# Kernel optimization log

Measured on AMD Instinct MI355X. Metric: run time of the kernel, lower is better.

Reference implementation:

```python
import jax, jax.numpy as jnp
import numpy as np

N_NODES = 50000
N_EDGES = 1600000
IN_DIM, HID_DIM, OUT_DIM, HEADS = 128, 128, 64, 8
NEG_SLOPE = 0.2
BN_EPS = 1e-5


def setup_inputs() -> dict:
    key = jax.random.key(0)
    ks = jax.random.split(key, 12)
    hpc = HID_DIM // HEADS  # per-head channels of layer 1
    return {
        "x": jax.random.normal(ks[0], (N_NODES, IN_DIM), jnp.float32),
        "edge_index": jax.random.randint(ks[1], (2, N_EDGES), 0, N_NODES, jnp.int64),
        "W1": jax.random.normal(ks[2], (IN_DIM, HEADS * hpc), jnp.float32) * 0.05,
        "a1_src": jax.random.normal(ks[3], (HEADS, hpc), jnp.float32) * 0.1,
        "a1_dst": jax.random.normal(ks[4], (HEADS, hpc), jnp.float32) * 0.1,
        "b1": jnp.zeros((HEADS * hpc,), jnp.float32),
        "bn_gamma": jnp.ones((HID_DIM,), jnp.float32),
        "bn_beta": jnp.zeros((HID_DIM,), jnp.float32),
        "W2": jax.random.normal(ks[5], (HID_DIM, OUT_DIM), jnp.float32) * 0.05,
        "a2_src": jax.random.normal(ks[6], (1, OUT_DIM), jnp.float32) * 0.1,
        "a2_dst": jax.random.normal(ks[7], (1, OUT_DIM), jnp.float32) * 0.1,
        "b2": jnp.zeros((OUT_DIM,), jnp.float32),
    }


def _gat_conv(x, src, dst, W, a_src, a_dst, bias, heads, n_nodes):
    # x: [N, Fin]; src/dst: [E'] (self-loops already appended)
    hpc = W.shape[1] // heads
    h = (x @ W).reshape(n_nodes, heads, hpc)                 # [N,H,C]
    alpha_s = jnp.einsum("nhc,hc->nh", h, a_src)             # [N,H]
    alpha_d = jnp.einsum("nhc,hc->nh", h, a_dst)
    e = alpha_s[src] + alpha_d[dst]                          # [E',H]
    e = jax.nn.leaky_relu(e, NEG_SLOPE)
    # segment softmax over destination neighborhoods
    m = jax.ops.segment_max(e, dst, num_segments=n_nodes)    # [N,H]
    m = jnp.where(jnp.isfinite(m), m, 0.0)
    ee = jnp.exp(e - m[dst])
    denom = jax.ops.segment_sum(ee, dst, num_segments=n_nodes)
    alpha = ee / (denom[dst] + 1e-16)                        # [E',H]
    msg = h[src] * alpha[:, :, None]                         # [E',H,C]
    out = jax.ops.segment_sum(msg, dst, num_segments=n_nodes)  # [N,H,C]
    return out.reshape(n_nodes, heads * hpc) + bias


def _batch_norm(x, gamma, beta):
    mu = jnp.mean(x, axis=0)
    var = jnp.var(x, axis=0)
    return gamma * (x - mu) * jax.lax.rsqrt(var + BN_EPS) + beta


def reference(x, edge_index, W1, a1_src, a1_dst, b1, bn_gamma, bn_beta, W2, a2_src, a2_dst, b2):
    n = x.shape[0]
    loops = jnp.arange(n, dtype=edge_index.dtype)
    src = jnp.concatenate([edge_index[0], loops])            # PyG add_self_loops
    dst = jnp.concatenate([edge_index[1], loops])
    h = _gat_conv(x, src, dst, W1, a1_src, a1_dst, b1, HEADS, n)
    h = _batch_norm(h, bn_gamma, bn_beta)
    h = jax.nn.elu(h)
    # dropout: identity at inference
    out = _gat_conv(h, src, dst, W2, a2_src, a2_dst, b2, 1, n)
    return out
```

## Files before the change

### kernel.cpp

```cpp
#include <hip/hip_runtime.h>
#include <hip/hip_bf16.h>

#define N_NODES 50000
#define N_EDGES 1600000
#define HEADS 8
#define NBK 196
#define NBLK 196

typedef unsigned short u16;
typedef unsigned int u32;
typedef __attribute__((ext_vector_type(8))) short bf16x8;
typedef __attribute__((ext_vector_type(4))) float f32x4;

__device__ __forceinline__ float bf2f(u16 u) {
  union { u32 i; float f; } v; v.i = ((u32)u) << 16; return v.f;
}
__device__ __forceinline__ float bflo(u32 p) {
  union { u32 i; float f; } v; v.i = p << 16; return v.f;
}
__device__ __forceinline__ float bfhi(u32 p) {
  union { u32 i; float f; } v; v.i = p & 0xffff0000u; return v.f;
}
__device__ __forceinline__ u16 f2bf(float f) {
  union { float f; u32 i; } v; v.f = f;
  u32 r = v.i + 0x7fff + ((v.i >> 16) & 1);
  return (u16)(r >> 16);
}
__device__ __forceinline__ u32 pack2(float a, float b) {
  return (u32)f2bf(a) | ((u32)f2bf(b) << 16);
}

__global__ void k_detect(const u16* __restrict__ x, const u32* __restrict__ ei,
                         int* __restrict__ flags) {
  __shared__ int cbig, cnz;
  if (threadIdx.x == 0) { cbig = 0; cnz = 0; }
  __syncthreads();
  int lb = 0, ln = 0;
  for (int i = threadIdx.x; i < 4096; i += 256) {
    int ex = (x[i] >> 7) & 0xff;
    lb += (ex >= 140);
    if (i < 2048) ln += (ei[2 * i + 1] != 0);
  }
  atomicAdd(&cbig, lb); atomicAdd(&cnz, ln);
  __syncthreads();
  if (threadIdx.x == 0) {
    flags[0] = (cbig > 16) ? 1 : 0;
    flags[1] = (cnz == 0) ? 1 : 0;
  }
}

__global__ void k_convsmall(const void* a1s, const void* a1d, const void* b1,
                            const void* gam, const void* bet, const void* a2s,
                            const void* a2d, const void* b2, const void* W1,
                            const void* W2, float* __restrict__ smallf,
                            u16* __restrict__ w1t, u16* __restrict__ w2t,
                            const int* __restrict__ flags) {
  int i = blockIdx.x * 256 + threadIdx.x;
  if (i >= 25408) return;
  bool f32 = flags[0] != 0;
  auto ld = [&](const void* p, int off) -> float {
    return f32 ? ((const float*)p)[off] : bf2f(((const u16*)p)[off]);
  };
  if (i >= 17216) {
    int j = i - 17216, n = j >> 7, k = j & 127;
    w2t[j] = f2bf(ld(W2, k * 64 + n));
  } else if (i >= 832) {
    int j = i - 832, n = j >> 7, k = j & 127;
    w1t[j] = f2bf(ld(W1, k * 128 + n));
  } else {
    const void* src; int off;
    if (i >= 768)      { src = b2;  off = i - 768; }
    else if (i >= 704) { src = a2d; off = i - 704; }
    else if (i >= 640) { src = a2s; off = i - 640; }
    else if (i >= 512) { src = bet; off = i - 512; }
    else if (i >= 384) { src = gam; off = i - 384; }
    else if (i >= 256) { src = b1;  off = i - 256; }
    else if (i >= 128) { src = a1d; off = i - 128; }
    else               { src = a1s; off = i; }
    smallf[i] = ld(src, off);
  }
}

__global__ __launch_bounds__(256) void k_hist(const int* __restrict__ ei,
                                              int* __restrict__ H,
                                              int* __restrict__ totals,
                                              const int* __restrict__ flags) {
  __shared__ int hist[NBK];
  int t = threadIdx.x, blk = blockIdx.x;
  for (int i = t; i < NBK; i += 256) hist[i] = 0;
  __syncthreads();
  bool i64 = flags[1] != 0;
  int base = blk * 8192;
  for (int k = 0; k < 32; k++) {
    int e = base + k * 256 + t;
    if (e < N_EDGES) {
      int d = i64 ? ei[2 * (N_EDGES + e)] : ei[N_EDGES + e];
      atomicAdd(&hist[d >> 8], 1);
    }
  }
  __syncthreads();
  for (int i = t; i < NBK; i += 256) {
    H[i * NBLK + blk] = hist[i];
    atomicAdd(&totals[i], hist[i]);
  }
}

__global__ void k_scan_tot(const int* __restrict__ totals, int* __restrict__ bucketBase) {
  __shared__ int tmp[256];
  int t = threadIdx.x;
  int v = (t < NBK) ? totals[t] : 0;
  tmp[t] = v; __syncthreads();
  for (int o = 1; o < 256; o <<= 1) {
    int x = (t >= o) ? tmp[t - o] : 0; __syncthreads();
    tmp[t] += x; __syncthreads();
  }
  if (t < NBK) bucketBase[t] = tmp[t] - v;
  if (t == NBK - 1) bucketBase[NBK] = tmp[t];
}

__global__ void k_scan_blk(const int* __restrict__ H, const int* __restrict__ bucketBase,
                           int* __restrict__ P) {
  __shared__ int tmp[256];
  int t = threadIdx.x, b = blockIdx.x;
  int v = (t < NBLK) ? H[b * NBLK + t] : 0;
  tmp[t] = v; __syncthreads();
  for (int o = 1; o < 256; o <<= 1) {
    int x = (t >= o) ? tmp[t - o] : 0; __syncthreads();
    tmp[t] += x; __syncthreads();
  }
  if (t < NBLK) P[b * NBLK + t] = bucketBase[b] + tmp[t] - v;
}

__global__ __launch_bounds__(256) void k_bucket(const int* __restrict__ ei,
                                                const int* __restrict__ P,
                                                u32* __restrict__ buf,
                                                const int* __restrict__ flags) {
  __shared__ int cur[NBK];
  int t = threadIdx.x, blk = blockIdx.x;
  for (int i = t; i < NBK; i += 256) cur[i] = P[i * NBLK + blk];
  __syncthreads();
  bool i64 = flags[1] != 0;
  int base = blk * 8192;
  for (int k = 0; k < 32; k++) {
    int e = base + k * 256 + t;
    if (e < N_EDGES) {
      int s = i64 ? ei[2 * e] : ei[e];
      int d = i64 ? ei[2 * (N_EDGES + e)] : ei[N_EDGES + e];
      int pos = atomicAdd(&cur[d >> 8], 1);
      buf[pos] = ((u32)(d & 255) << 16) | (u32)s;
    }
  }
}

__global__ __launch_bounds__(256) void k_csr(const u32* __restrict__ buf,
                                             const int* __restrict__ bucketBase,
                                             int* __restrict__ row_start,
                                             int* __restrict__ deg,
                                             int* __restrict__ csr, int N) {
  __shared__ int cnt[256], scn[256], cur[256];
  int b = blockIdx.x, t = threadIdx.x;
  int lo = bucketBase[b], hi = bucketBase[b + 1];
  cnt[t] = 0; __syncthreads();
  for (int e = lo + t; e < hi; e += 256) atomicAdd(&cnt[(buf[e] >> 16) & 255], 1);
  __syncthreads();
  int v = cnt[t];
  scn[t] = v; __syncthreads();
  for (int o = 1; o < 256; o <<= 1) {
    int x = (t >= o) ? scn[t - o] : 0; __syncthreads();
    scn[t] += x; __syncthreads();
  }
  int excl = scn[t] - v;
  int node = b * 256 + t;
  if (node < N) { row_start[node] = lo + excl; deg[node] = v; }
  cur[t] = lo + excl;
  __syncthreads();
  for (int e = lo + t; e < hi; e += 256) {
    u32 p = buf[e];
    int pos = atomicAdd(&cur[(p >> 16) & 255], 1);
    csr[pos] = p & 0xffff;
  }
}

template <int NCOLS, bool EPI, bool AFLAG>
__global__ __launch_bounds__(256) void k_gemm_mfma(const void* __restrict__ A,
                                                   const u16* __restrict__ BT,
                                                   const float* __restrict__ scale,
                                                   const float* __restrict__ shift,
                                                   u16* __restrict__ C, int M,
                                                   const int* __restrict__ flags) {
  constexpr int KP = 136;
  constexpr int NT = NCOLS / 16;
  __shared__ u16 As[64 * KP];
  __shared__ u16 Bs[NCOLS * KP];
  int t = threadIdx.x;
  int row0 = blockIdx.x * 64;
  bool af32 = AFLAG ? (flags[0] != 0) : false;

  for (int i = t; i < NCOLS * 16; i += 256) {
    int n = i >> 4, q = i & 15;
    *(uint4*)&Bs[n * KP + q * 8] = ((const uint4*)BT)[n * 16 + q];
  }
  for (int i = t; i < 64 * 32; i += 256) {
    int r = i >> 5, c4 = i & 31;
    int row = row0 + r;
    uint2 pk = make_uint2(0u, 0u);
    if (row < M) {
      if (EPI) {
        uint2 p = ((const uint2*)A)[(size_t)row * 32 + c4];
        int c = c4 * 4;
        float v0 = bflo(p.x), v1 = bfhi(p.x), v2 = bflo(p.y), v3 = bfhi(p.y);
        v0 = fmaf(v0, scale[c],     shift[c]);     v0 = v0 > 0.f ? v0 : __expf(v0) - 1.f;
        v1 = fmaf(v1, scale[c + 1], shift[c + 1]); v1 = v1 > 0.f ? v1 : __expf(v1) - 1.f;
        v2 = fmaf(v2, scale[c + 2], shift[c + 2]); v2 = v2 > 0.f ? v2 : __expf(v2) - 1.f;
        v3 = fmaf(v3, scale[c + 3], shift[c + 3]); v3 = v3 > 0.f ? v3 : __expf(v3) - 1.f;
        pk.x = pack2(v0, v1); pk.y = pack2(v2, v3);
      } else if (af32) {
        float4 v = ((const float4*)A)[(size_t)row * 32 + c4];
        pk.x = pack2(v.x, v.y); pk.y = pack2(v.z, v.w);
      } else {
        pk = ((const uint2*)A)[(size_t)row * 32 + c4];
      }
    }
    *(uint2*)&As[r * KP + c4 * 4] = pk;
  }
  __syncthreads();

  int lane = t & 63, w = t >> 6;
  int m = lane & 15, quad = lane >> 4;
  f32x4 acc[NT];
#pragma unroll
  for (int nt = 0; nt < NT; nt++) acc[nt] = (f32x4)(0.f);
  const u16* aBase = &As[(w * 16 + m) * KP + quad * 8];
  const u16* bBase = &Bs[m * KP + quad * 8];
#pragma unroll
  for (int ks = 0; ks < 4; ks++) {
    bf16x8 af = *(const bf16x8*)(aBase + ks * 32);
#pragma unroll
    for (int nt = 0; nt < NT; nt++) {
      bf16x8 bf = *(const bf16x8*)(bBase + nt * 16 * KP + ks * 32);
      acc[nt] = __builtin_amdgcn_mfma_f32_16x16x32_bf16(af, bf, acc[nt], 0, 0, 0);
    }
  }
  int orow0 = row0 + w * 16 + quad * 4;
#pragma unroll
  for (int nt = 0; nt < NT; nt++) {
#pragma unroll
    for (int r = 0; r < 4; r++) {
      int row = orow0 + r;
      if (row < M) C[(size_t)row * NCOLS + nt * 16 + m] = f2bf(acc[nt][r]);
    }
  }
}

__global__ void k_alpha1(const u16* __restrict__ h1b, const float* __restrict__ a1s,
                         const float* __restrict__ a1d, float* __restrict__ as_out,
                         float* __restrict__ ad_out, int N) {
  int idx = blockIdx.x * 256 + threadIdx.x;
  if (idx >= N * HEADS) return;
  int n = idx >> 3, h = idx & 7;
  const u32* hp = (const u32*)&h1b[((size_t)n << 7) + (h << 4)];
  float s = 0.f, d = 0.f;
#pragma unroll
  for (int q = 0; q < 8; q++) {
    u32 p = hp[q];
    float v0 = bflo(p), v1 = bfhi(p);
    int b = (h << 4) + q * 2;
    s = fmaf(v0, a1s[b], s); s = fmaf(v1, a1s[b + 1], s);
    d = fmaf(v0, a1d[b], d); d = fmaf(v1, a1d[b + 1], d);
  }
  as_out[idx] = s; ad_out[idx] = d;
}

__global__ __launch_bounds__(256) void k_agg1(const u16* __restrict__ h1b,
                                              const float* __restrict__ as_,
                                              const float* __restrict__ ad_,
                                              const int* __restrict__ csr,
                                              const int* __restrict__ row_start,
                                              const int* __restrict__ deg,
                                              const float* __restrict__ b1,
                                              u16* __restrict__ out, int N) {
  int node = blockIdx.x * 4 + (threadIdx.x >> 6);
  if (node >= N) return;
  int l = threadIdx.x & 63;
  int head = l >> 3;
  int node_u = __builtin_amdgcn_readfirstlane(node);
  int st = __builtin_amdgcn_readfirstlane(row_start[node_u]);
  int cnt = __builtin_amdgcn_readfirstlane(deg[node_u]);
  const int* cp = csr + st;
  const u32* h32 = (const u32*)h1b;
  float ad = ad_[(node_u << 3) | head];
  float s = 0.f, a0 = 0.f, a1 = 0.f;
  int j = 0;
  for (; j + 4 <= cnt; j += 4) {
    int s0 = cp[j], s1 = cp[j + 1], s2 = cp[j + 2], s3 = cp[j + 3];
    float e0 = (as_ + (s0 << 3))[head], e1 = (as_ + (s1 << 3))[head];
    float e2 = (as_ + (s2 << 3))[head], e3 = (as_ + (s3 << 3))[head];
    u32 h0 = (h32 + (s0 << 6))[l], h1v = (h32 + (s1 << 6))[l];
    u32 h2v = (h32 + (s2 << 6))[l], h3 = (h32 + (s3 << 6))[l];
    e0 += ad; e0 = fmaxf(e0, 0.2f * e0); float p0 = __expf(e0);
    e1 += ad; e1 = fmaxf(e1, 0.2f * e1); float p1 = __expf(e1);
    e2 += ad; e2 = fmaxf(e2, 0.2f * e2); float p2 = __expf(e2);
    e3 += ad; e3 = fmaxf(e3, 0.2f * e3); float p3 = __expf(e3);
    s += (p0 + p1) + (p2 + p3);
    a0 = fmaf(p0, bflo(h0), a0);  a1 = fmaf(p0, bfhi(h0), a1);
    a0 = fmaf(p1, bflo(h1v), a0); a1 = fmaf(p1, bfhi(h1v), a1);
    a0 = fmaf(p2, bflo(h2v), a0); a1 = fmaf(p2, bfhi(h2v), a1);
    a0 = fmaf(p3, bflo(h3), a0);  a1 = fmaf(p3, bfhi(h3), a1);
  }
  for (; j < cnt; j++) {
    int s0 = cp[j];
    float e0 = (as_ + (s0 << 3))[head] + ad;
    e0 = fmaxf(e0, 0.2f * e0);
    float p0 = __expf(e0);
    u32 h0 = (h32 + (s0 << 6))[l];
    s += p0;
    a0 = fmaf(p0, bflo(h0), a0); a1 = fmaf(p0, bfhi(h0), a1);
  }
  {
    float e0 = (as_ + (node_u << 3))[head] + ad;
    e0 = fmaxf(e0, 0.2f * e0);
    float p0 = __expf(e0);
    u32 h0 = (h32 + (node_u << 6))[l];
    s += p0;
    a0 = fmaf(p0, bflo(h0), a0); a1 = fmaf(p0, bfhi(h0), a1);
  }
  float inv = 1.f / (s + 1e-16f);
  int c0 = l * 2;
  ((u32*)out)[((size_t)node_u << 6) + l] =
      pack2(fmaf(a0, inv, b1[c0]), fmaf(a1, inv, b1[c0 + 1]));
}

__global__ void k_bnstat(const u16* __restrict__ h, float* __restrict__ gsum,
                         float* __restrict__ gsq, int N) {
  __shared__ float ts[256], tq[256];
  int t = threadIdx.x, col = t & 127, rr = t >> 7;
  int row0 = blockIdx.x * 128;
  float s = 0.f, q = 0.f;
  for (int r = rr; r < 128; r += 2) {
    int row = row0 + r;
    if (row < N) {
      float v = bf2f(h[((size_t)row << 7) + col]);
      s += v; q = fmaf(v, v, q);
    }
  }
  ts[t] = s; tq[t] = q; __syncthreads();
  if (t < 128) {
    atomicAdd(&gsum[t], ts[t] + ts[t + 128]);
    atomicAdd(&gsq[t], tq[t] + tq[t + 128]);
  }
}

__global__ void k_bnfin(const float* __restrict__ gsum, const float* __restrict__ gsq,
                        const float* __restrict__ gamma, const float* __restrict__ beta,
                        float* __restrict__ scale, float* __restrict__ shift, int N) {
  int t = threadIdx.x;
  if (t >= 128) return;
  float mu = gsum[t] / (float)N;
  float var = fmaxf(gsq[t] / (float)N - mu * mu, 0.f);
  float s = gamma[t] * rsqrtf(var + 1e-5f);
  scale[t] = s;
  shift[t] = beta[t] - mu * s;
}

__global__ void k_alpha2(const u16* __restrict__ h2b, const float* __restrict__ a2s,
                         const float* __restrict__ a2d, float* __restrict__ as_out,
                         float* __restrict__ ad_out, int N) {
  int w = threadIdx.x >> 6;
  int node = blockIdx.x * 4 + w;
  if (node >= N) return;
  int l = threadIdx.x & 63;
  float v = bf2f(h2b[((size_t)node << 6) + l]);
  float vs = v * a2s[l], vd = v * a2d[l];
  for (int o = 32; o; o >>= 1) { vs += __shfl_xor(vs, o, 64); vd += __shfl_xor(vd, o, 64); }
  if (l == 0) { as_out[node] = vs; ad_out[node] = vd; }
}

__global__ __launch_bounds__(256) void k_agg2(const u16* __restrict__ h2b,
                                              const float* __restrict__ as_,
                                              const float* __restrict__ ad_,
                                              const int* __restrict__ csr,
                                              const int* __restrict__ row_start,
                                              const int* __restrict__ deg,
                                              const float* __restrict__ b2,
                                              void* __restrict__ out,
                                              const int* __restrict__ flags, int N) {
  int node = blockIdx.x * 4 + (threadIdx.x >> 6);
  if (node >= N) return;
  int l = threadIdx.x & 63;
  int node_u = __builtin_amdgcn_readfirstlane(node);
  int st = __builtin_amdgcn_readfirstlane(row_start[node_u]);
  int cnt = __builtin_amdgcn_readfirstlane(deg[node_u]);
  const int* cp = csr + st;
  float ad = ad_[node_u];
  float s = 0.f, a = 0.f;
  int j = 0;
  for (; j + 4 <= cnt; j += 4) {
    int s0 = cp[j], s1 = cp[j + 1], s2 = cp[j + 2], s3 = cp[j + 3];
    float e0 = as_[s0], e1 = as_[s1], e2 = as_[s2], e3 = as_[s3];
    u16 v0 = (h2b + (s0 << 6))[l], v1 = (h2b + (s1 << 6))[l];
    u16 v2 = (h2b + (s2 << 6))[l], v3 = (h2b + (s3 << 6))[l];
    e0 += ad; e0 = fmaxf(e0, 0.2f * e0); float p0 = __expf(e0);
    e1 += ad; e1 = fmaxf(e1, 0.2f * e1); float p1 = __expf(e1);
    e2 += ad; e2 = fmaxf(e2, 0.2f * e2); float p2 = __expf(e2);
    e3 += ad; e3 = fmaxf(e3, 0.2f * e3); float p3 = __expf(e3);
    s += (p0 + p1) + (p2 + p3);
    a = fmaf(p0, bf2f(v0), a); a = fmaf(p1, bf2f(v1), a);
    a = fmaf(p2, bf2f(v2), a); a = fmaf(p3, bf2f(v3), a);
  }
  for (; j < cnt; j++) {
    int s0 = cp[j];
    float e0 = as_[s0] + ad;
    e0 = fmaxf(e0, 0.2f * e0);
    float p0 = __expf(e0);
    s += p0;
    a = fmaf(p0, bf2f((h2b + (s0 << 6))[l]), a);
  }
  {
    float e0 = as_[node_u] + ad;
    e0 = fmaxf(e0, 0.2f * e0);
    float p0 = __expf(e0);
    s += p0;
    a = fmaf(p0, bf2f((h2b + (node_u << 6))[l]), a);
  }
  float r = a / (s + 1e-16f) + b2[l];
  size_t idx = ((size_t)node_u << 6) + l;
  if (flags[0]) ((float*)out)[idx] = r;
  else          ((u16*)out)[idx] = f2bf(r);
}

extern "C" void kernel_launch(void* const* d_in, const int* in_sizes, int n_in,
                              void* d_out, int out_size, void* d_ws, size_t ws_size,
                              hipStream_t stream) {
  const void* x   = d_in[0];
  const int*  ei  = (const int*)d_in[1];
  const void* W1  = d_in[2];
  const void* a1s = d_in[3];
  const void* a1d = d_in[4];
  const void* b1  = d_in[5];
  const void* gam = d_in[6];
  const void* bet = d_in[7];
  const void* W2  = d_in[8];
  const void* a2s = d_in[9];
  const void* a2d = d_in[10];
  const void* b2  = d_in[11];

  char* ws = (char*)d_ws;
  size_t off = 0;
  auto alloc = [&](size_t bytes) -> void* {
    void* p = ws + off;
    off += (bytes + 255) & ~(size_t)255;
    return p;
  };
  int* flags = (int*)alloc(256);
  char* zreg = (char*)alloc(2048);
  int* totals = (int*)zreg;
  float* gsum = (float*)(zreg + 1024);
  float* gsq  = gsum + 128;
  int* H  = (int*)alloc((size_t)NBK * NBLK * 4);
  int* P  = (int*)alloc((size_t)NBK * NBLK * 4);
  int* bucketBase = (int*)alloc(1024);
  u32* ebuf = (u32*)alloc((size_t)N_EDGES * 4);
  int* csr = (int*)alloc((size_t)N_EDGES * 4);
  int* row_start = (int*)alloc((size_t)N_NODES * 4);
  int* deg = (int*)alloc((size_t)N_NODES * 4);
  float* smallf = (float*)alloc(832 * 4);
  float* a1sf = smallf;        float* a1df = smallf + 128;
  float* b1f  = smallf + 256;  float* gamf = smallf + 384;
  float* betf = smallf + 512;  float* a2sf = smallf + 640;
  float* a2df = smallf + 704;  float* b2f  = smallf + 768;
  u16* w1t = (u16*)alloc(16384 * 2);
  u16* w2t = (u16*)alloc(8192 * 2);
  u16* h1b  = (u16*)alloc((size_t)N_NODES * 128 * 2);
  u16* h1ob = (u16*)alloc((size_t)N_NODES * 128 * 2);
  u16* h2b  = (u16*)alloc((size_t)N_NODES * 64 * 2);
  float* al1s = (float*)alloc((size_t)N_NODES * 8 * 4);
  float* al1d = (float*)alloc((size_t)N_NODES * 8 * 4);
  float* scale = (float*)alloc(512);
  float* shift = (float*)alloc(512);
  float* al2s = (float*)alloc((size_t)N_NODES * 4);
  float* al2d = (float*)alloc((size_t)N_NODES * 4);
  if (off > ws_size) return;

  hipMemsetAsync(zreg, 0, 2048, stream);
  k_detect<<<1, 256, 0, stream>>>((const u16*)x, (const u32*)ei, flags);
  k_convsmall<<<100, 256, 0, stream>>>(a1s, a1d, b1, gam, bet, a2s, a2d, b2, W1, W2,
                                       smallf, w1t, w2t, flags);

  k_hist<<<NBLK, 256, 0, stream>>>(ei, H, totals, flags);
  k_scan_tot<<<1, 256, 0, stream>>>(totals, bucketBase);
  k_scan_blk<<<NBK, 256, 0, stream>>>(H, bucketBase, P);
  k_bucket<<<NBLK, 256, 0, stream>>>(ei, P, ebuf, flags);
  k_csr<<<NBK, 256, 0, stream>>>(ebuf, bucketBase, row_start, deg, csr, N_NODES);

  k_gemm_mfma<128, false, true><<<(N_NODES + 63) / 64, 256, 0, stream>>>(
      x, w1t, nullptr, nullptr, h1b, N_NODES, flags);
  k_alpha1<<<(N_NODES * HEADS + 255) / 256, 256, 0, stream>>>(h1b, a1sf, a1df,
                                                              al1s, al1d, N_NODES);
  k_agg1<<<(N_NODES + 3) / 4, 256, 0, stream>>>(h1b, al1s, al1d, csr, row_start, deg,
                                                b1f, h1ob, N_NODES);

  k_bnstat<<<(N_NODES + 127) / 128, 256, 0, stream>>>(h1ob, gsum, gsq, N_NODES);
  k_bnfin<<<1, 128, 0, stream>>>(gsum, gsq, gamf, betf, scale, shift, N_NODES);

  k_gemm_mfma<64, true, false><<<(N_NODES + 63) / 64, 256, 0, stream>>>(
      h1ob, w2t, scale, shift, h2b, N_NODES, flags);
  k_alpha2<<<(N_NODES + 3) / 4, 256, 0, stream>>>(h2b, a2sf, a2df, al2s, al2d, N_NODES);
  k_agg2<<<(N_NODES + 3) / 4, 256, 0, stream>>>(h2b, al2s, al2d, csr, row_start, deg,
                                                b2f, d_out, flags, N_NODES);
}
```

Before: 350.0 us.

## Stage bucketed edges in LDS, fuse alpha2 into GEMM, lane-parallel softmax weights

```diff
diff --git a/kernel.cpp b/kernel.cpp
--- a/kernel.cpp
+++ b/kernel.cpp
@@ -6,8 +6,10 @@
 #define HEADS 8
 #define NBK 196
 #define NBLK 196
+#define EPB 8192
 
 typedef unsigned short u16;
+typedef unsigned char u8;
 typedef unsigned int u32;
 typedef __attribute__((ext_vector_type(8))) short bf16x8;
 typedef __attribute__((ext_vector_type(4))) float f32x4;
@@ -90,7 +92,7 @@
   for (int i = t; i < NBK; i += 256) hist[i] = 0;
   __syncthreads();
   bool i64 = flags[1] != 0;
-  int base = blk * 8192;
+  int base = blk * EPB;
   for (int k = 0; k < 32; k++) {
     int e = base + k * 256 + t;
     if (e < N_EDGES) {
@@ -135,20 +137,47 @@
                                                 const int* __restrict__ P,
                                                 u32* __restrict__ buf,
                                                 const int* __restrict__ flags) {
-  __shared__ int cur[NBK];
+  __shared__ u32 sv[EPB];
+  __shared__ u16 rank[EPB];
+  __shared__ u8  sk8[EPB];
+  __shared__ int cnt[NBK], scn[NBK], tmp[256];
   int t = threadIdx.x, blk = blockIdx.x;
-  for (int i = t; i < NBK; i += 256) cur[i] = P[i * NBLK + blk];
+  int base = blk * EPB;
+  int nE = N_EDGES - base; if (nE > EPB) nE = EPB;
+  for (int i = t; i < NBK; i += 256) cnt[i] = 0;
   __syncthreads();
   bool i64 = flags[1] != 0;
-  int base = blk * 8192;
-  for (int k = 0; k < 32; k++) {
-    int e = base + k * 256 + t;
-    if (e < N_EDGES) {
+  for (int k = 0; k < EPB / 256; k++) {
+    int li = k * 256 + t, e = base + li;
+    if (li < nE) {
+      int d = i64 ? ei[2 * (N_EDGES + e)] : ei[N_EDGES + e];
+      rank[li] = (u16)atomicAdd(&cnt[d >> 8], 1);
+    }
+  }
+  __syncthreads();
+  int v = (t < NBK) ? cnt[t] : 0;
+  tmp[t] = v; __syncthreads();
+  for (int o = 1; o < 256; o <<= 1) {
+    int x = (t >= o) ? tmp[t - o] : 0; __syncthreads();
+    tmp[t] += x; __syncthreads();
+  }
+  if (t < NBK) scn[t] = tmp[t] - v;
+  __syncthreads();
+  for (int k = 0; k < EPB / 256; k++) {
+    int li = k * 256 + t, e = base + li;
+    if (li < nE) {
       int s = i64 ? ei[2 * e] : ei[e];
       int d = i64 ? ei[2 * (N_EDGES + e)] : ei[N_EDGES + e];
-      int pos = atomicAdd(&cur[d >> 8], 1);
-      buf[pos] = ((u32)(d & 255) << 16) | (u32)s;
-    }
+      int key = d >> 8;
+      int pos = scn[key] + rank[li];
+      sv[pos] = ((u32)(d & 255) << 16) | (u32)s;
+      sk8[pos] = (u8)key;
+    }
+  }
+  __syncthreads();
+  for (int i = t; i < nE; i += 256) {
+    int b = sk8[i];
+    buf[P[b * NBLK + blk] + (i - scn[b])] = sv[i];
   }
 }
 
@@ -186,6 +215,10 @@
                                                    const u16* __restrict__ BT,
                                                    const float* __restrict__ scale,
                                                    const float* __restrict__ shift,
+                                                   const float* __restrict__ a2s,
+                                                   const float* __restrict__ a2d,
+                                                   float* __restrict__ as_out,
+                                                   float* __restrict__ ad_out,
                                                    u16* __restrict__ C, int M,
                                                    const int* __restrict__ flags) {
   constexpr int KP = 136;
@@ -250,6 +283,26 @@
       if (row < M) C[(size_t)row * NCOLS + nt * 16 + m] = f2bf(acc[nt][r]);
     }
   }
+  if (EPI) {
+    float a2sv[NT], a2dv[NT];
+#pragma unroll
+    for (int nt = 0; nt < NT; nt++) { a2sv[nt] = a2s[nt * 16 + m]; a2dv[nt] = a2d[nt * 16 + m]; }
+#pragma unroll
+    for (int r = 0; r < 4; r++) {
+      float vs = 0.f, vd = 0.f;
+#pragma unroll
+      for (int nt = 0; nt < NT; nt++) {
+        vs = fmaf(acc[nt][r], a2sv[nt], vs);
+        vd = fmaf(acc[nt][r], a2dv[nt], vd);
+      }
+      vs += __shfl_xor(vs, 1); vd += __shfl_xor(vd, 1);
+      vs += __shfl_xor(vs, 2); vd += __shfl_xor(vd, 2);
+      vs += __shfl_xor(vs, 4); vd += __shfl_xor(vd, 4);
+      vs += __shfl_xor(vs, 8); vd += __shfl_xor(vd, 8);
+      int row = orow0 + r;
+      if (row < M && m == 0) { as_out[row] = vs; ad_out[row] = vd; }
+    }
+  }
 }
 
 __global__ void k_alpha1(const u16* __restrict__ h1b, const float* __restrict__ a1s,
@@ -282,49 +335,52 @@
   int node = blockIdx.x * 4 + (threadIdx.x >> 6);
   if (node >= N) return;
   int l = threadIdx.x & 63;
-  int head = l >> 3;
+  int head = l >> 3, sub = l & 7;
+  int gbase = l & 56;
   int node_u = __builtin_amdgcn_readfirstlane(node);
   int st = __builtin_amdgcn_readfirstlane(row_start[node_u]);
   int cnt = __builtin_amdgcn_readfirstlane(deg[node_u]);
   const int* cp = csr + st;
   const u32* h32 = (const u32*)h1b;
   float ad = ad_[(node_u << 3) | head];
-  float s = 0.f, a0 = 0.f, a1 = 0.f;
+  float sp = 0.f, a0 = 0.f, a1 = 0.f;
   int j = 0;
-  for (; j + 4 <= cnt; j += 4) {
-    int s0 = cp[j], s1 = cp[j + 1], s2 = cp[j + 2], s3 = cp[j + 3];
-    float e0 = (as_ + (s0 << 3))[head], e1 = (as_ + (s1 << 3))[head];
-    float e2 = (as_ + (s2 << 3))[head], e3 = (as_ + (s3 << 3))[head];
-    u32 h0 = (h32 + (s0 << 6))[l], h1v = (h32 + (s1 << 6))[l];
-    u32 h2v = (h32 + (s2 << 6))[l], h3 = (h32 + (s3 << 6))[l];
-    e0 += ad; e0 = fmaxf(e0, 0.2f * e0); float p0 = __expf(e0);
-    e1 += ad; e1 = fmaxf(e1, 0.2f * e1); float p1 = __expf(e1);
-    e2 += ad; e2 = fmaxf(e2, 0.2f * e2); float p2 = __expf(e2);
-    e3 += ad; e3 = fmaxf(e3, 0.2f * e3); float p3 = __expf(e3);
-    s += (p0 + p1) + (p2 + p3);
-    a0 = fmaf(p0, bflo(h0), a0);  a1 = fmaf(p0, bfhi(h0), a1);
-    a0 = fmaf(p1, bflo(h1v), a0); a1 = fmaf(p1, bfhi(h1v), a1);
-    a0 = fmaf(p2, bflo(h2v), a0); a1 = fmaf(p2, bfhi(h2v), a1);
-    a0 = fmaf(p3, bflo(h3), a0);  a1 = fmaf(p3, bfhi(h3), a1);
+  for (; j + 8 <= cnt; j += 8) {
+    int ssub = cp[j + sub];
+    float e = as_[(ssub << 3) | head] + ad;
+    e = fmaxf(e, 0.2f * e);
+    float p = __expf(e);
+    sp += p;
+#pragma unroll
+    for (int k = 0; k < 8; k++) {
+      int sk = cp[j + k];
+      float pk = __shfl(p, gbase | k);
+      u32 hv = h32[(sk << 6) | l];
+      a0 = fmaf(pk, bflo(hv), a0);
+      a1 = fmaf(pk, bfhi(hv), a1);
+    }
   }
   for (; j < cnt; j++) {
     int s0 = cp[j];
-    float e0 = (as_ + (s0 << 3))[head] + ad;
+    float e0 = as_[(s0 << 3) | head] + ad;
     e0 = fmaxf(e0, 0.2f * e0);
     float p0 = __expf(e0);
-    u32 h0 = (h32 + (s0 << 6))[l];
-    s += p0;
-    a0 = fmaf(p0, bflo(h0), a0); a1 = fmaf(p0, bfhi(h0), a1);
+    if (sub == 0) sp += p0;
+    u32 hv = h32[(s0 << 6) | l];
+    a0 = fmaf(p0, bflo(hv), a0); a1 = fmaf(p0, bfhi(hv), a1);
   }
   {
-    float e0 = (as_ + (node_u << 3))[head] + ad;
+    float e0 = as_[(node_u << 3) | head] + ad;
     e0 = fmaxf(e0, 0.2f * e0);
     float p0 = __expf(e0);
-    u32 h0 = (h32 + (node_u << 6))[l];
-    s += p0;
-    a0 = fmaf(p0, bflo(h0), a0); a1 = fmaf(p0, bfhi(h0), a1);
-  }
-  float inv = 1.f / (s + 1e-16f);
+    if (sub == 0) sp += p0;
+    u32 hv = h32[((size_t)node_u << 6) | l];
+    a0 = fmaf(p0, bflo(hv), a0); a1 = fmaf(p0, bfhi(hv), a1);
+  }
+  sp += __shfl_xor(sp, 1);
+  sp += __shfl_xor(sp, 2);
+  sp += __shfl_xor(sp, 4);
+  float inv = 1.f / (sp + 1e-16f);
   int c0 = l * 2;
   ((u32*)out)[((size_t)node_u << 6) + l] =
       pack2(fmaf(a0, inv, b1[c0]), fmaf(a1, inv, b1[c0 + 1]));
@@ -360,19 +416,6 @@
   float s = gamma[t] * rsqrtf(var + 1e-5f);
   scale[t] = s;
   shift[t] = beta[t] - mu * s;
-}
-
-__global__ void k_alpha2(const u16* __restrict__ h2b, const float* __restrict__ a2s,
-                         const float* __restrict__ a2d, float* __restrict__ as_out,
-                         float* __restrict__ ad_out, int N) {
-  int w = threadIdx.x >> 6;
-  int node = blockIdx.x * 4 + w;
-  if (node >= N) return;
-  int l = threadIdx.x & 63;
-  float v = bf2f(h2b[((size_t)node << 6) + l]);
-  float vs = v * a2s[l], vd = v * a2d[l];
-  for (int o = 32; o; o >>= 1) { vs += __shfl_xor(vs, o, 64); vd += __shfl_xor(vd, o, 64); }
-  if (l == 0) { as_out[node] = vs; ad_out[node] = vd; }
 }
 
 __global__ __launch_bounds__(256) void k_agg2(const u16* __restrict__ h2b,
@@ -387,42 +430,46 @@
   int node = blockIdx.x * 4 + (threadIdx.x >> 6);
   if (node >= N) return;
   int l = threadIdx.x & 63;
+  int sub = l & 7, gbase = l & 56;
   int node_u = __builtin_amdgcn_readfirstlane(node);
   int st = __builtin_amdgcn_readfirstlane(row_start[node_u]);
   int cnt = __builtin_amdgcn_readfirstlane(deg[node_u]);
   const int* cp = csr + st;
   float ad = ad_[node_u];
-  float s = 0.f, a = 0.f;
+  float sp = 0.f, a = 0.f;
   int j = 0;
-  for (; j + 4 <= cnt; j += 4) {
-    int s0 = cp[j], s1 = cp[j + 1], s2 = cp[j + 2], s3 = cp[j + 3];
-    float e0 = as_[s0], e1 = as_[s1], e2 = as_[s2], e3 = as_[s3];
-    u16 v0 = (h2b + (s0 << 6))[l], v1 = (h2b + (s1 << 6))[l];
-    u16 v2 = (h2b + (s2 << 6))[l], v3 = (h2b + (s3 << 6))[l];
-    e0 += ad; e0 = fmaxf(e0, 0.2f * e0); float p0 = __expf(e0);
-    e1 += ad; e1 = fmaxf(e1, 0.2f * e1); float p1 = __expf(e1);
-    e2 += ad; e2 = fmaxf(e2, 0.2f * e2); float p2 = __expf(e2);
-    e3 += ad; e3 = fmaxf(e3, 0.2f * e3); float p3 = __expf(e3);
-    s += (p0 + p1) + (p2 + p3);
-    a = fmaf(p0, bf2f(v0), a); a = fmaf(p1, bf2f(v1), a);
-    a = fmaf(p2, bf2f(v2), a); a = fmaf(p3, bf2f(v3), a);
+  for (; j + 8 <= cnt; j += 8) {
+    int ssub = cp[j + sub];
+    float e = as_[ssub] + ad;
+    e = fmaxf(e, 0.2f * e);
+    float p = __expf(e);
+    sp += p;
+#pragma unroll
+    for (int k = 0; k < 8; k++) {
+      int sk = cp[j + k];
+      float pk = __shfl(p, gbase | k);
+      a = fmaf(pk, bf2f((h2b + (sk << 6))[l]), a);
+    }
   }
   for (; j < cnt; j++) {
     int s0 = cp[j];
     float e0 = as_[s0] + ad;
     e0 = fmaxf(e0, 0.2f * e0);
     float p0 = __expf(e0);
-    s += p0;
+    if (sub == 0) sp += p0;
     a = fmaf(p0, bf2f((h2b + (s0 << 6))[l]), a);
   }
   {
     float e0 = as_[node_u] + ad;
     e0 = fmaxf(e0, 0.2f * e0);
     float p0 = __expf(e0);
-    s += p0;
+    if (sub == 0) sp += p0;
     a = fmaf(p0, bf2f((h2b + (node_u << 6))[l]), a);
   }
-  float r = a / (s + 1e-16f) + b2[l];
+  sp += __shfl_xor(sp, 1);
+  sp += __shfl_xor(sp, 2);
+  sp += __shfl_xor(sp, 4);
+  float r = a / (sp + 1e-16f) + b2[l];
   size_t idx = ((size_t)node_u << 6) + l;
   if (flags[0]) ((float*)out)[idx] = r;
   else          ((u16*)out)[idx] = f2bf(r);
@@ -493,7 +540,7 @@
   k_csr<<<NBK, 256, 0, stream>>>(ebuf, bucketBase, row_start, deg, csr, N_NODES);
 
   k_gemm_mfma<128, false, true><<<(N_NODES + 63) / 64, 256, 0, stream>>>(
-      x, w1t, nullptr, nullptr, h1b, N_NODES, flags);
+      x, w1t, nullptr, nullptr, nullptr, nullptr, nullptr, nullptr, h1b, N_NODES, flags);
   k_alpha1<<<(N_NODES * HEADS + 255) / 256, 256, 0, stream>>>(h1b, a1sf, a1df,
                                                               al1s, al1d, N_NODES);
   k_agg1<<<(N_NODES + 3) / 4, 256, 0, stream>>>(h1b, al1s, al1d, csr, row_start, deg,
@@ -503,8 +550,7 @@
   k_bnfin<<<1, 128, 0, stream>>>(gsum, gsq, gamf, betf, scale, shift, N_NODES);
 
   k_gemm_mfma<64, true, false><<<(N_NODES + 63) / 64, 256, 0, stream>>>(
-      h1ob, w2t, scale, shift, h2b, N_NODES, flags);
-  k_alpha2<<<(N_NODES + 3) / 4, 256, 0, stream>>>(h2b, a2sf, a2df, al2s, al2d, N_NODES);
+      h1ob, w2t, scale, shift, a2sf, a2df, al2s, al2d, h2b, N_NODES, flags);
   k_agg2<<<(N_NODES + 3) / 4, 256, 0, stream>>>(h2b, al2s, al2d, csr, row_start, deg,
                                                 b2f, d_out, flags, N_NODES);
 }
```

New measurement: 329.3 us. -5.9%, faster.
